# Kernel tuning notes

Hardware: AMD Instinct MI355X
Metric: run time of the kernel (lower is better)

Reference implementation:

```python
import jax, jax.numpy as jnp
import numpy as np

HEADS = 4
BN_EPS = 1e-5


def _hgat_conv(x, src, dst, node_type, edge_attr, edge_type,
               ne, W, We, a_src, a_dst, a_edge, ee, Wres, b, concat):
    """Heterogeneous GAT conv: per-type embeddings + edge-featured attention.
    x: [N, Fin]; edge_attr: [E, De]; returns [N, H*C] (concat) or [N, C]."""
    N = x.shape[0]
    C = W.shape[1] // HEADS
    xi = x + ne[node_type]                                  # node-type conditioning
    h = (xi @ W).reshape(N, HEADS, C)                       # [N, H, C]
    he = ((edge_attr + ee[edge_type]) @ We).reshape(-1, HEADS, C)  # [E, H, C]
    s = jnp.einsum('nhc,hc->nh', h, a_src)                  # [N, H]
    d = jnp.einsum('nhc,hc->nh', h, a_dst)                  # [N, H]
    e = jnp.einsum('ehc,hc->eh', he, a_edge)                # [E, H]
    alpha = jax.nn.leaky_relu(s[src] + d[dst] + e, 0.2)     # [E, H]
    # softmax over incoming edges per destination node
    amax = jax.ops.segment_max(alpha, dst, num_segments=N)  # [N, H]
    amax = jnp.where(jnp.isfinite(amax), amax, 0.0)
    ex = jnp.exp(alpha - amax[dst])
    den = jax.ops.segment_sum(ex, dst, num_segments=N)
    coef = ex / (den[dst] + 1e-16)                          # [E, H]
    msg = h[src] * coef[:, :, None]                         # [E, H, C]
    out = jax.ops.segment_sum(msg, dst, num_segments=N)     # [N, H, C]
    out = out.reshape(N, HEADS * C) if concat else out.mean(axis=1)
    return out + x @ Wres + b                               # residual + bias


def _batch_norm(x, gamma, beta):
    mu = x.mean(axis=0)
    var = x.var(axis=0)
    return (x - mu) * jax.lax.rsqrt(var + BN_EPS) * gamma + beta


def setup_inputs() -> dict:
    key = jax.random.key(0)
    ks = jax.random.split(key, 32)
    N, E, H = 50000, 400000, 32          # nodes, edges, hidden_channels
    DE = 64                               # edge_dim
    NT, ET = 3, 4                         # node / edge type counts
    D1 = H * HEADS                        # 128 = enc1 output / enc2 width

    def g(k, shape, scale=1.0):
        return (jax.random.normal(ks[k], shape, dtype=jnp.float32) * scale)

    inp = {
        'x': g(0, (N, H)),
        'edge_index': jax.random.randint(ks[1], (2, E), 0, N, dtype=jnp.int32),
        'node_type': jax.random.randint(ks[2], (N,), 0, NT, dtype=jnp.int32),
        'edge_attr': g(3, (E, DE)),
        'edge_type': jax.random.randint(ks[4], (E,), 0, ET, dtype=jnp.int32),
        # enc1 params (in=32, per-head out=32, concat -> 128)
        'ne1': g(5, (NT, H), 0.1),
        'w1': g(6, (H, HEADS * H), 1.0 / np.sqrt(H)),
        'we1': g(7, (DE, HEADS * H), 1.0 / np.sqrt(DE)),
        'asrc1': g(8, (HEADS, H), 0.1), 'adst1': g(9, (HEADS, H), 0.1),
        'aedge1': g(10, (HEADS, H), 0.1),
        'ee1': g(11, (ET, DE), 0.1),
        'wres1': g(12, (H, D1), 1.0 / np.sqrt(H)),
        'b1': jnp.zeros((D1,), jnp.float32),
        # BatchNorm(128)
        'gamma': jnp.ones((D1,), jnp.float32),
        'beta': jnp.zeros((D1,), jnp.float32),
        # enc2 params (in=128, per-head out=128, mean -> 128)
        'ne2': g(13, (NT, D1), 0.1),
        'w2': g(14, (D1, HEADS * D1), 1.0 / np.sqrt(D1)),
        'we2': g(15, (DE, HEADS * D1), 1.0 / np.sqrt(DE)),
        'asrc2': g(16, (HEADS, D1), 0.1), 'adst2': g(17, (HEADS, D1), 0.1),
        'aedge2': g(18, (HEADS, D1), 0.1),
        'ee2': g(19, (ET, DE), 0.1),
        'wres2': g(20, (D1, D1), 1.0 / np.sqrt(D1)),
        'b2': jnp.zeros((D1,), jnp.float32),
    }
    return inp


def reference(x, edge_index, node_type, edge_attr, edge_type,
              ne1, w1, we1, asrc1, adst1, aedge1, ee1, wres1, b1,
              gamma, beta,
              ne2, w2, we2, asrc2, adst2, aedge2, ee2, wres2, b2):
    src, dst = edge_index[0], edge_index[1]
    h = _hgat_conv(x, src, dst, node_type, edge_attr, edge_type,
                   ne1, w1, we1, asrc1, adst1, aedge1, ee1, wres1, b1,
                   concat=True)
    h = _batch_norm(h, gamma, beta)
    out = _hgat_conv(h, src, dst, node_type, edge_attr, edge_type,
                     ne2, w2, we2, asrc2, adst2, aedge2, ee2, wres2, b2,
                     concat=False)
    return out
```

## Files before the change

### kernel.cpp

```cpp
#include <hip/hip_runtime.h>
#include <hip/hip_bf16.h>

typedef unsigned short u16;
typedef unsigned int u32;

constexpr int NN = 50000;
constexpr int NE = 400000;
constexpr int MPAD = 50048;

typedef __attribute__((ext_vector_type(8))) short s16x8;
typedef __attribute__((ext_vector_type(4))) float f32x4;

__device__ __forceinline__ float bf2f(u16 u) {
    union { u32 i; float f; } v; v.i = ((u32)u) << 16; return v.f;
}
__device__ __forceinline__ u16 f2bf(float f) {
    union { float f; u32 i; } v; v.f = f;
    u32 r = v.i + 0x7fffu + ((v.i >> 16) & 1u);
    return (u16)(r >> 16);
}
__device__ __forceinline__ float ldf(const void* p, size_t i, int isbf) {
    if (isbf) return bf2f(((const u16*)p)[i]);
    return ((const float*)p)[i];
}
__device__ __forceinline__ float clampf(float v) {
    return fminf(fmaxf(v, -1e4f), 1e4f);
}

__device__ int   g_flag;
__device__ int   g_counter;
__device__ float g_qe1[256], g_qe2[256];
__device__ float g_ps1[128], g_pd1[128], g_ps2[512], g_pd2[512];
__device__ float g_bnsum[128], g_bnsumsq[128], g_bnscale[128], g_bnshift[128];
__device__ int   g_deg[NN], g_start[NN], g_cur[NN];
__device__ int   g_eidx[NE];
__device__ __attribute__((aligned(16))) float g_sbuf[NN * 4];
__device__ __attribute__((aligned(16))) float g_dbuf[NN * 4];
__device__ __attribute__((aligned(16))) float g_alpha[(size_t)NE * 4];
__device__ __attribute__((aligned(16))) float g_xbuf[(size_t)NN * 128];
__device__ __attribute__((aligned(16))) float g_acc2[(size_t)NN * 128];
__device__ __attribute__((aligned(16))) u16 g_A1[(size_t)MPAD * 64];
__device__ __attribute__((aligned(16))) u16 g_A2[(size_t)MPAD * 160];
__device__ __attribute__((aligned(16))) u16 g_B1t[192 * 64];
__device__ __attribute__((aligned(16))) u16 g_B1bt[128 * 128];
__device__ __attribute__((aligned(16))) u16 g_B2t[192 * 160];
__device__ __attribute__((aligned(16))) u16 g_B2bt[128 * 512];
__device__ __attribute__((aligned(16))) u16 g_xi1[(size_t)NN * 32];
__device__ __attribute__((aligned(16))) u16 g_xi2[(size_t)NN * 128];
__device__ __attribute__((aligned(16))) u16 g_agg1[(size_t)MPAD * 128];
__device__ __attribute__((aligned(16))) u16 g_agg2[(size_t)MPAD * 512];

__global__ void k_detect(const u16* x) {
    if (threadIdx.x == 0) {
        int cnt = 0;
        for (int i = 0; i < 64; i++) {
            u16 u = x[2 * i];
            int ex = (u >> 7) & 0xff;
            if (ex >= 100 && ex <= 140) cnt++;
        }
        g_flag = (cnt >= 40) ? 1 : 0;
        g_counter = 0;
    }
}
__global__ void k_zero() {
    int i = blockIdx.x * blockDim.x + threadIdx.x;
    if (i < NN) g_deg[i] = 0;
    if (i < 128) { g_bnsum[i] = 0.f; g_bnsumsq[i] = 0.f; }
}

__global__ __launch_bounds__(256) void k_prep(
    const void* we1, const void* ae1, const void* we2, const void* ae2,
    const void* w1, const void* as1, const void* ad1,
    const void* w2, const void* as2, const void* ad2) {
    int isbf = g_flag;
    int t = threadIdx.x;
    int idx = blockIdx.x * 16 + (t >> 4);
    int s = t & 15;
    float a = 0.f;
    if (idx < 256) {
        int k = idx >> 2, hd = idx & 3;
        for (int c = s; c < 32; c += 16)
            a += ldf(we1, k * 128 + hd * 32 + c, isbf) * ldf(ae1, hd * 32 + c, isbf);
    } else if (idx < 512) {
        int i2 = idx - 256;
        int k = i2 >> 2, hd = i2 & 3;
        for (int c = s; c < 128; c += 16)
            a += ldf(we2, k * 512 + hd * 128 + c, isbf) * ldf(ae2, hd * 128 + c, isbf);
    } else if (idx < 768) {
        int i2 = idx - 512;
        int isd = i2 >> 7, j = i2 & 127;
        int h = j >> 5, k = j & 31;
        const void* av = isd ? ad1 : as1;
        for (int c = s; c < 32; c += 16)
            a += ldf(w1, k * 128 + h * 32 + c, isbf) * ldf(av, h * 32 + c, isbf);
    } else {
        int i2 = idx - 768;
        int isd = i2 >> 9, j = i2 & 511;
        int h = j >> 7, k = j & 127;
        const void* av = isd ? ad2 : as2;
        for (int c = s; c < 128; c += 16)
            a += ldf(w2, (size_t)k * 512 + h * 128 + c, isbf) * ldf(av, h * 128 + c, isbf);
    }
#pragma unroll
    for (int mk = 8; mk >= 1; mk >>= 1) a += __shfl_xor(a, mk);
    if (s == 0) {
        if (idx < 256) g_qe1[idx] = a;
        else if (idx < 512) g_qe2[idx - 256] = a;
        else if (idx < 768) {
            int i2 = idx - 512;
            if (i2 >> 7) g_pd1[i2 & 127] = a; else g_ps1[i2 & 127] = a;
        } else {
            int i2 = idx - 768;
            if (i2 >> 9) g_pd2[i2 & 511] = a; else g_ps2[i2 & 511] = a;
        }
    }
}

__global__ void k_deg(const int* __restrict__ dstp) {
    int e = blockIdx.x * blockDim.x + threadIdx.x;
    if (e < NE) atomicAdd(&g_deg[dstp[e]], 1);
}
__global__ void k_start() {
    int n = blockIdx.x * blockDim.x + threadIdx.x;
    if (n < NN) {
        int d = g_deg[n];
        int s = atomicAdd(&g_counter, d);
        g_start[n] = s; g_cur[n] = s;
    }
}
__global__ void k_scatter(const int* __restrict__ dstp) {
    int e = blockIdx.x * blockDim.x + threadIdx.x;
    if (e < NE) {
        int slot = atomicAdd(&g_cur[dstp[e]], 1);
        g_eidx[slot] = e;
    }
}

__device__ __forceinline__ u16 a1val(const void* x, int n, int k, int nt, int isbf) {
    if (k < 32) return f2bf(ldf(x, (size_t)n * 32 + k, isbf));
    if (k == 32 + nt || k == 35) return 0x3F80u;
    return 0;
}
__global__ __launch_bounds__(256) void k_buildA1(const void* x, const int* __restrict__ ntype,
                                                 const void* ne1) {
    int isbf = g_flag;
    int i = blockIdx.x * 256 + threadIdx.x;
    if (i >= MPAD * 32) return;
    int n = i >> 5, k2 = (i & 31) << 1;
    u32 pk = 0;
    if (n < NN) {
        int nt = ntype[n];
        pk = (u32)a1val(x, n, k2, nt, isbf) | ((u32)a1val(x, n, k2 + 1, nt, isbf) << 16);
        if (k2 < 32) {
            float x0 = ldf(x, (size_t)n * 32 + k2, isbf) + ldf(ne1, nt * 32 + k2, isbf);
            float x1 = ldf(x, (size_t)n * 32 + k2 + 1, isbf) + ldf(ne1, nt * 32 + k2 + 1, isbf);
            ((u32*)g_xi1)[(size_t)n * 16 + (k2 >> 1)] =
                (u32)f2bf(x0) | ((u32)f2bf(x1) << 16);
        }
    }
    ((u32*)g_A1)[i] = pk;
}
__global__ __launch_bounds__(256) void k_a2tail(const int* __restrict__ ntype) {
    int i = blockIdx.x * 256 + threadIdx.x;
    if (i >= NN * 16) return;
    int n = i >> 4, q = i & 15;
    int k2 = 128 + q * 2;
    int nt = ntype[n];
    u16 lo = (k2 == 128 + nt || k2 == 131) ? 0x3F80u : 0;
    u16 hi = (k2 + 1 == 128 + nt || k2 + 1 == 131) ? 0x3F80u : 0;
    ((u32*)g_A2)[(size_t)n * 80 + 64 + q] = (u32)lo | ((u32)hi << 16);
}
__global__ __launch_bounds__(256) void k_xi2(const int* __restrict__ ntype, const void* ne2) {
    int isbf = g_flag;
    int i = blockIdx.x * 256 + threadIdx.x;
    if (i >= NN * 64) return;
    int n = i >> 6, jp = (i & 63) << 1;
    int nt = ntype[n];
    float v0 = g_xbuf[(size_t)n * 128 + jp] * g_bnscale[jp] + g_bnshift[jp]
             + ldf(ne2, nt * 128 + jp, isbf);
    float v1 = g_xbuf[(size_t)n * 128 + jp + 1] * g_bnscale[jp + 1] + g_bnshift[jp + 1]
             + ldf(ne2, nt * 128 + jp + 1, isbf);
    ((u32*)g_xi2)[i] = (u32)f2bf(v0) | ((u32)f2bf(v1) << 16);
}

__global__ void k_buildB1(const void* ne1, const void* w1, const void* wres1, const void* b1) {
    int isbf = g_flag;
    int j = blockIdx.x;
    int k = threadIdx.x;
    float v = 0.f;
    if (j < 128) {
        if (k < 32) v = ldf(wres1, k * 128 + j, isbf);
        else if (k == 35) v = ldf(b1, j, isbf);
    } else if (j < 136) {
        int h = (j - 128) & 3;
        const float* p = (j < 132) ? g_ps1 : g_pd1;
        if (k < 32) v = p[h * 32 + k];
        else if (k < 35) {
            int tt = k - 32; float a = 0.f;
            for (int c = 0; c < 32; c++)
                a += ldf(ne1, tt * 32 + c, isbf) * p[h * 32 + c];
            v = a;
        }
    }
    (void)w1;
    g_B1t[j * 64 + k] = f2bf(v);
}
__global__ void k_buildB1b(const void* w1) {
    int isbf = g_flag;
    int j = blockIdx.x;
    int k = threadIdx.x;
    float v = ((k >> 5) == (j >> 5)) ? ldf(w1, (k & 31) * 128 + j, isbf) : 0.f;
    g_B1bt[j * 128 + k] = f2bf(v);
}
__global__ void k_buildB2(const void* ne2, const void* w2, const void* wres2, const void* b2) {
    int isbf = g_flag;
    int j = blockIdx.x;
    int k = threadIdx.x;
    if (k >= 160) return;
    float v = 0.f;
    if (j < 128) {
        if (k < 128) v = g_bnscale[k] * ldf(wres2, k * 128 + j, isbf);
        else if (k == 131) {
            float a = ldf(b2, j, isbf);
            for (int c = 0; c < 128; c++)
                a += g_bnshift[c] * ldf(wres2, c * 128 + j, isbf);
            v = a;
        }
    } else if (j < 136) {
        int h = (j - 128) & 3;
        const float* p = (j < 132) ? g_ps2 : g_pd2;
        if (k < 128) v = g_bnscale[k] * p[h * 128 + k];
        else if (k < 131) {
            int tt = k - 128; float a = 0.f;
            for (int c = 0; c < 128; c++)
                a += (g_bnshift[c] + ldf(ne2, tt * 128 + c, isbf)) * p[h * 128 + c];
            v = a;
        }
    }
    (void)w2;
    g_B2t[j * 160 + k] = f2bf(v);
}
__global__ void k_buildB2b(const void* w2) {
    int isbf = g_flag;
    int j = blockIdx.x;
    for (int k = threadIdx.x; k < 512; k += 256) {
        float v = 0.25f * ldf(w2, (size_t)(k & 127) * 512 + (k >> 7) * 128 + j, isbf);
        g_B2bt[j * 512 + k] = f2bf(v);
    }
}

template<int K, int KT, int LAYER>
__global__ __launch_bounds__(256) void k_gemm(void* outp) {
    constexpr int KP = KT + 8;
    __shared__ __attribute__((aligned(16))) u16 As[64 * KP];
    __shared__ __attribute__((aligned(16))) u16 Bs[64 * KP];
    const u16* __restrict__ A  = (LAYER == 1) ? g_A1 : (LAYER == 2) ? g_A2
                               : (LAYER == 3) ? g_agg1 : g_agg2;
    const u16* __restrict__ Bt = (LAYER == 1) ? g_B1t : (LAYER == 2) ? g_B2t
                               : (LAYER == 3) ? g_B1bt : g_B2bt;
    int isbf = g_flag;
    const int t = threadIdx.x;
    const int mb = blockIdx.x, cb = blockIdx.y;
    const int wave = t >> 6, lane = t & 63;
    const int lr = lane & 15, lg = lane >> 4;
    f32x4 acc[4] = {};
    constexpr int CH = KT / 8;
#pragma unroll 1
    for (int kt = 0; kt < K / KT; kt++) {
        __syncthreads();
        for (int c = t; c < 64 * CH; c += 256) {
            int r = c / CH, o = (c - r * CH) * 8;
            *(s16x8*)&As[r * KP + o] =
                *(const s16x8*)&A[((size_t)(mb * 64 + r)) * K + kt * KT + o];
            *(s16x8*)&Bs[r * KP + o] =
                *(const s16x8*)&Bt[((size_t)(cb * 64 + r)) * K + kt * KT + o];
        }
        __syncthreads();
        const u16* ap  = &As[(wave * 16 + lr) * KP + lg * 8];
        const u16* bp0 = &Bs[lr * KP + lg * 8];
#pragma unroll
        for (int ks = 0; ks < KT / 32; ks++) {
            s16x8 af = *(const s16x8*)(ap + ks * 32);
#pragma unroll
            for (int ct = 0; ct < 4; ct++) {
                s16x8 bf = *(const s16x8*)(bp0 + ct * 16 * KP + ks * 32);
                acc[ct] = __builtin_amdgcn_mfma_f32_16x16x32_bf16(af, bf, acc[ct], 0, 0, 0);
            }
        }
    }
    const int rowb = mb * 64 + wave * 16 + lg * 4;
#pragma unroll
    for (int ct = 0; ct < 4; ct++) {
        int j = cb * 64 + ct * 16 + lr;
#pragma unroll
        for (int r = 0; r < 4; r++) {
            int n = rowb + r;
            if (n >= NN) continue;
            float v = acc[ct][r];
            if (LAYER == 1) {
                if (j < 128)      g_xbuf[(size_t)n * 128 + j] = clampf(v);
                else if (j < 132) g_sbuf[n * 4 + (j - 128)] = clampf(v);
                else if (j < 136) g_dbuf[n * 4 + (j - 132)] = clampf(v);
            } else if (LAYER == 2) {
                if (j < 128)      g_acc2[(size_t)n * 128 + j] = clampf(v);
                else if (j < 132) g_sbuf[n * 4 + (j - 128)] = clampf(v);
                else if (j < 136) g_dbuf[n * 4 + (j - 132)] = clampf(v);
            } else if (LAYER == 3) {
                float* p = &g_xbuf[(size_t)n * 128 + j];
                float x = clampf(*p + v);
                *p = x;
                g_A2[(size_t)n * 160 + j] = f2bf(x);
            } else {
                float v2 = clampf(g_acc2[(size_t)n * 128 + j] + v);
                if (isbf) ((u16*)outp)[(size_t)n * 128 + j] = f2bf(v2);
                else      ((float*)outp)[(size_t)n * 128 + j] = v2;
            }
        }
    }
}

__global__ __launch_bounds__(256) void k_edge(
    const int* __restrict__ srcp, const int* __restrict__ dstp,
    const int* __restrict__ etype, const void* eattr,
    const void* ee, int lyr) {
    __shared__ float eel[4 * 68];
    __shared__ float qel[256];
    int isbf = g_flag;
    int t = threadIdx.x;
    const float* qe = (lyr == 1) ? g_qe1 : g_qe2;
    { int tt = t >> 6, k = t & 63; eel[tt * 68 + k] = ldf(ee, tt * 64 + k, isbf); }
    qel[t] = qe[t];
    __syncthreads();
    int sub = t & 15;
    float q[4][4];
#pragma unroll
    for (int i = 0; i < 4; i++)
#pragma unroll
        for (int h = 0; h < 4; h++)
            q[i][h] = qel[(sub * 4 + i) * 4 + h];
    int g = t >> 4;
    int e = blockIdx.x * 16 + g;
    if (e >= NE) return;
    int et = etype[e];
    float ev[4];
    if (isbf) {
        ushort4 vv = *(const ushort4*)((const u16*)eattr + (size_t)e * 64 + sub * 4);
        ev[0] = bf2f(vv.x); ev[1] = bf2f(vv.y); ev[2] = bf2f(vv.z); ev[3] = bf2f(vv.w);
    } else {
        float4 vv = *(const float4*)((const float*)eattr + (size_t)e * 64 + sub * 4);
        ev[0] = vv.x; ev[1] = vv.y; ev[2] = vv.z; ev[3] = vv.w;
    }
    const float* ep = eel + et * 68 + sub * 4;
    float p0 = 0.f, p1 = 0.f, p2 = 0.f, p3 = 0.f;
#pragma unroll
    for (int i = 0; i < 4; i++) {
        float evi = ev[i] + ep[i];
        p0 += evi * q[i][0]; p1 += evi * q[i][1];
        p2 += evi * q[i][2]; p3 += evi * q[i][3];
    }
#pragma unroll
    for (int mk = 1; mk < 16; mk <<= 1) {
        p0 += __shfl_xor(p0, mk); p1 += __shfl_xor(p1, mk);
        p2 += __shfl_xor(p2, mk); p3 += __shfl_xor(p3, mk);
    }
    if (sub == 0) {
        int ss = srcp[e], dd = dstp[e];
        float4 sb = *(const float4*)(g_sbuf + ss * 4);
        float4 db = *(const float4*)(g_dbuf + dd * 4);
        float a0 = sb.x + db.x + p0;
        float a1 = sb.y + db.y + p1;
        float a2 = sb.z + db.z + p2;
        float a3 = sb.w + db.w + p3;
        a0 = a0 > 0.f ? a0 : 0.2f * a0;
        a1 = a1 > 0.f ? a1 : 0.2f * a1;
        a2 = a2 > 0.f ? a2 : 0.2f * a2;
        a3 = a3 > 0.f ? a3 : 0.2f * a3;
        *(float4*)(g_alpha + 4 * (size_t)e) = make_float4(
            clampf(a0), clampf(a1), clampf(a2), clampf(a3));
    }
}

__global__ __launch_bounds__(256) void k_att1(const int* __restrict__ srcp) {
    int lane = threadIdx.x & 63;
    int n = blockIdx.x * 4 + (threadIdx.x >> 6);
    if (n >= NN) return;
    int st = g_start[n], dg = g_deg[n];
    float m0 = -1e30f, m1 = -1e30f, m2 = -1e30f, m3 = -1e30f;
    for (int i = lane; i < dg; i += 64) {
        int e = g_eidx[st + i];
        float4 a = *(const float4*)(g_alpha + 4 * (size_t)e);
        m0 = fmaxf(m0, a.x); m1 = fmaxf(m1, a.y);
        m2 = fmaxf(m2, a.z); m3 = fmaxf(m3, a.w);
    }
    for (int mk = 32; mk >= 1; mk >>= 1) {
        m0 = fmaxf(m0, __shfl_xor(m0, mk)); m1 = fmaxf(m1, __shfl_xor(m1, mk));
        m2 = fmaxf(m2, __shfl_xor(m2, mk)); m3 = fmaxf(m3, __shfl_xor(m3, mk));
    }
    int j0 = 2 * lane;
    int hd = j0 >> 5;
    float z0 = 0.f, z1 = 0.f, z2 = 0.f, z3 = 0.f;
    float acc0 = 0.f, acc1 = 0.f;
    for (int base = 0; base < dg; base += 64) {
        int i = base + lane;
        int sidx = 0; float c0 = 0.f, c1 = 0.f, c2 = 0.f, c3 = 0.f;
        if (i < dg) {
            int e = g_eidx[st + i];
            float4 a = *(const float4*)(g_alpha + 4 * (size_t)e);
            sidx = srcp[e];
            c0 = expf(a.x - m0); c1 = expf(a.y - m1);
            c2 = expf(a.z - m2); c3 = expf(a.w - m3);
            z0 += c0; z1 += c1; z2 += c2; z3 += c3;
        }
        int cnt = min(64, dg - base);
        for (int jj = 0; jj < cnt; jj++) {
            int s2 = __shfl(sidx, jj);
            float b0 = __shfl(c0, jj), b1 = __shfl(c1, jj);
            float b2v = __shfl(c2, jj), b3 = __shfl(c3, jj);
            float cs = hd == 0 ? b0 : hd == 1 ? b1 : hd == 2 ? b2v : b3;
            u32 hv = *(const u32*)(g_xi1 + (size_t)s2 * 32 + (j0 & 31));
            acc0 += bf2f((u16)(hv & 0xffff)) * cs;
            acc1 += bf2f((u16)(hv >> 16)) * cs;
        }
    }
    for (int mk = 32; mk >= 1; mk >>= 1) {
        z0 += __shfl_xor(z0, mk); z1 += __shfl_xor(z1, mk);
        z2 += __shfl_xor(z2, mk); z3 += __shfl_xor(z3, mk);
    }
    float iv = 1.f / ((hd == 0 ? z0 : hd == 1 ? z1 : hd == 2 ? z2 : z3) + 1e-16f);
    ((u32*)g_agg1)[((size_t)n * 128 + j0) >> 1] =
        (u32)f2bf(acc0 * iv) | ((u32)f2bf(acc1 * iv) << 16);
}

__global__ __launch_bounds__(256) void k_bnstats() {
    int t = threadIdx.x;
    int j = t & 127;
    int r0 = blockIdx.x * 2 + (t >> 7);
    float s = 0.f, ss = 0.f;
    for (int r = r0; r < NN; r += 500) {
        float v = g_xbuf[(size_t)r * 128 + j];
        s += v; ss += v * v;
    }
    atomicAdd(&g_bnsum[j], s);
    atomicAdd(&g_bnsumsq[j], ss);
}
__global__ void k_bnfin(const void* gamma, const void* beta) {
    int isbf = g_flag;
    int j = threadIdx.x;
    float mu = g_bnsum[j] * (1.f / NN);
    float var = fmaxf(g_bnsumsq[j] * (1.f / NN) - mu * mu, 0.f);
    float rstd = rsqrtf(var + 1e-5f);
    float sc = ldf(gamma, j, isbf) * rstd;
    g_bnscale[j] = sc;
    g_bnshift[j] = ldf(beta, j, isbf) - mu * sc;
}

__global__ __launch_bounds__(256) void k_att2(const int* __restrict__ srcp) {
    int lane = threadIdx.x & 63;
    int n = blockIdx.x * 4 + (threadIdx.x >> 6);
    if (n >= NN) return;
    int st = g_start[n], dg = g_deg[n];
    float m0 = -1e30f, m1 = -1e30f, m2 = -1e30f, m3 = -1e30f;
    for (int i = lane; i < dg; i += 64) {
        int e = g_eidx[st + i];
        float4 a = *(const float4*)(g_alpha + 4 * (size_t)e);
        m0 = fmaxf(m0, a.x); m1 = fmaxf(m1, a.y);
        m2 = fmaxf(m2, a.z); m3 = fmaxf(m3, a.w);
    }
    for (int mk = 32; mk >= 1; mk >>= 1) {
        m0 = fmaxf(m0, __shfl_xor(m0, mk)); m1 = fmaxf(m1, __shfl_xor(m1, mk));
        m2 = fmaxf(m2, __shfl_xor(m2, mk)); m3 = fmaxf(m3, __shfl_xor(m3, mk));
    }
    int c0 = 2 * lane;
    float z0 = 0.f, z1 = 0.f, z2 = 0.f, z3 = 0.f;
    float a00 = 0.f, a01 = 0.f, a10 = 0.f, a11 = 0.f;
    float a20 = 0.f, a21 = 0.f, a30 = 0.f, a31 = 0.f;
    for (int base = 0; base < dg; base += 64) {
        int i = base + lane;
        int sidx = 0; float c0f = 0.f, c1f = 0.f, c2f = 0.f, c3f = 0.f;
        if (i < dg) {
            int e = g_eidx[st + i];
            float4 a = *(const float4*)(g_alpha + 4 * (size_t)e);
            sidx = srcp[e];
            c0f = expf(a.x - m0); c1f = expf(a.y - m1);
            c2f = expf(a.z - m2); c3f = expf(a.w - m3);
            z0 += c0f; z1 += c1f; z2 += c2f; z3 += c3f;
        }
        int cnt = min(64, dg - base);
        for (int jj = 0; jj < cnt; jj++) {
            int s2 = __shfl(sidx, jj);
            float b0 = __shfl(c0f, jj), b1 = __shfl(c1f, jj);
            float b2v = __shfl(c2f, jj), b3 = __shfl(c3f, jj);
            u32 hv = *(const u32*)(g_xi2 + (size_t)s2 * 128 + c0);
            float lo = bf2f((u16)(hv & 0xffff)), hi = bf2f((u16)(hv >> 16));
            a00 += lo * b0;  a01 += hi * b0;
            a10 += lo * b1;  a11 += hi * b1;
            a20 += lo * b2v; a21 += hi * b2v;
            a30 += lo * b3;  a31 += hi * b3;
        }
    }
    for (int mk = 32; mk >= 1; mk >>= 1) {
        z0 += __shfl_xor(z0, mk); z1 += __shfl_xor(z1, mk);
        z2 += __shfl_xor(z2, mk); z3 += __shfl_xor(z3, mk);
    }
    float iv0 = 1.f / (z0 + 1e-16f), iv1 = 1.f / (z1 + 1e-16f);
    float iv2 = 1.f / (z2 + 1e-16f), iv3 = 1.f / (z3 + 1e-16f);
    u32* out = (u32*)g_agg2 + (((size_t)n * 512 + c0) >> 1);
    out[0]   = (u32)f2bf(a00 * iv0) | ((u32)f2bf(a01 * iv0) << 16);
    out[64]  = (u32)f2bf(a10 * iv1) | ((u32)f2bf(a11 * iv1) << 16);
    out[128] = (u32)f2bf(a20 * iv2) | ((u32)f2bf(a21 * iv2) << 16);
    out[192] = (u32)f2bf(a30 * iv3) | ((u32)f2bf(a31 * iv3) << 16);
}

extern "C" void kernel_launch(void* const* d_in, const int* in_sizes, int n_in,
                              void* d_out, int out_size, void* d_ws, size_t ws_size,
                              hipStream_t stream) {
    const void* x     = d_in[0];
    const int* ei     = (const int*)d_in[1];
    const int* ntype  = (const int*)d_in[2];
    const void* eattr = d_in[3];
    const int* etype  = (const int*)d_in[4];
    const void* ne1   = d_in[5];
    const void* w1    = d_in[6];
    const void* we1   = d_in[7];
    const void* asrc1 = d_in[8];
    const void* adst1 = d_in[9];
    const void* aedge1= d_in[10];
    const void* ee1   = d_in[11];
    const void* wres1 = d_in[12];
    const void* b1    = d_in[13];
    const void* gamma = d_in[14];
    const void* beta  = d_in[15];
    const void* ne2   = d_in[16];
    const void* w2    = d_in[17];
    const void* we2   = d_in[18];
    const void* asrc2 = d_in[19];
    const void* adst2 = d_in[20];
    const void* aedge2= d_in[21];
    const void* ee2   = d_in[22];
    const void* wres2 = d_in[23];
    const void* b2    = d_in[24];
    (void)in_sizes; (void)n_in; (void)out_size; (void)d_ws; (void)ws_size;

    const int* srcp = ei;
    const int* dstp = ei + NE;

    k_detect<<<1, 64, 0, stream>>>((const u16*)x);
    k_zero<<<196, 256, 0, stream>>>();
    k_prep<<<112, 256, 0, stream>>>(we1, aedge1, we2, aedge2,
                                    w1, asrc1, adst1, w2, asrc2, adst2);
    k_deg<<<1563, 256, 0, stream>>>(dstp);
    k_start<<<196, 256, 0, stream>>>();
    k_scatter<<<1563, 256, 0, stream>>>(dstp);

    k_buildA1<<<(MPAD * 32 + 255) / 256, 256, 0, stream>>>(x, ntype, ne1);
    k_buildB1<<<192, 64, 0, stream>>>(ne1, w1, wres1, b1);
    k_buildB1b<<<128, 128, 0, stream>>>(w1);
    k_gemm<64, 64, 1><<<dim3(MPAD / 64, 3), 256, 0, stream>>>(nullptr);
    k_edge<<<NE / 16, 256, 0, stream>>>(srcp, dstp, etype, eattr, ee1, 1);
    k_att1<<<12500, 256, 0, stream>>>(srcp);
    k_gemm<128, 128, 3><<<dim3(MPAD / 64, 2), 256, 0, stream>>>(nullptr);

    k_bnstats<<<250, 256, 0, stream>>>();
    k_bnfin<<<1, 128, 0, stream>>>(gamma, beta);

    k_xi2<<<12500, 256, 0, stream>>>(ntype, ne2);
    k_a2tail<<<(NN * 16 + 255) / 256, 256, 0, stream>>>(ntype);
    k_buildB2<<<192, 192, 0, stream>>>(ne2, w2, wres2, b2);
    k_buildB2b<<<128, 256, 0, stream>>>(w2);
    k_gemm<160, 160, 2><<<dim3(MPAD / 64, 3), 256, 0, stream>>>(nullptr);
    k_edge<<<NE / 16, 256, 0, stream>>>(srcp, dstp, etype, eattr, ee2, 2);
    k_att2<<<12500, 256, 0, stream>>>(srcp);
    k_gemm<512, 128, 4><<<dim3(MPAD / 64, 2), 256, 0, stream>>>(d_out);
}
```

Before: 620.8 us.

## Fuse aggregation with output GEMMs and share edge-feature pass across layers

The attention-aggregation kernels now write each block's 32 aggregated node rows into shared memory and immediately run the MFMA projection (W1 per head, or the mean-folded W2) on them. This removes the g_agg1/g_agg2 global round trips and the separate GEMM launches. Both layers' edge-attribute projections are computed in one pass over edge_attr, with the per-edge-type term precomputed into a 16-entry table. Layer 2 gets a light edge kernel that only adds the source and destination scores. The cost is a larger shared-memory footprint, lower occupancy in the fused kernels, and B-matrix reads straight from global memory.

```diff
diff --git a/kernel.cpp b/kernel.cpp
--- a/kernel.cpp
+++ b/kernel.cpp
@@ -30,6 +30,7 @@
 __device__ int   g_flag;
 __device__ int   g_counter;
 __device__ float g_qe1[256], g_qe2[256];
+__device__ float g_eq1[16], g_eq2[16];
 __device__ float g_ps1[128], g_pd1[128], g_ps2[512], g_pd2[512];
 __device__ float g_bnsum[128], g_bnsumsq[128], g_bnscale[128], g_bnshift[128];
 __device__ int   g_deg[NN], g_start[NN], g_cur[NN];
@@ -37,18 +38,17 @@
 __device__ __attribute__((aligned(16))) float g_sbuf[NN * 4];
 __device__ __attribute__((aligned(16))) float g_dbuf[NN * 4];
 __device__ __attribute__((aligned(16))) float g_alpha[(size_t)NE * 4];
+__device__ __attribute__((aligned(16))) float g_el2[(size_t)NE * 4];
 __device__ __attribute__((aligned(16))) float g_xbuf[(size_t)NN * 128];
 __device__ __attribute__((aligned(16))) float g_acc2[(size_t)NN * 128];
 __device__ __attribute__((aligned(16))) u16 g_A1[(size_t)MPAD * 64];
 __device__ __attribute__((aligned(16))) u16 g_A2[(size_t)MPAD * 160];
 __device__ __attribute__((aligned(16))) u16 g_B1t[192 * 64];
-__device__ __attribute__((aligned(16))) u16 g_B1bt[128 * 128];
+__device__ __attribute__((aligned(16))) u16 g_B1ct[128 * 32];
 __device__ __attribute__((aligned(16))) u16 g_B2t[192 * 160];
 __device__ __attribute__((aligned(16))) u16 g_B2bt[128 * 512];
 __device__ __attribute__((aligned(16))) u16 g_xi1[(size_t)NN * 32];
 __device__ __attribute__((aligned(16))) u16 g_xi2[(size_t)NN * 128];
-__device__ __attribute__((aligned(16))) u16 g_agg1[(size_t)MPAD * 128];
-__device__ __attribute__((aligned(16))) u16 g_agg2[(size_t)MPAD * 512];
 
 __global__ void k_detect(const u16* x) {
     if (threadIdx.x == 0) {
@@ -115,6 +115,24 @@
         }
     }
 }
+__global__ void k_prep2(const void* ee1, const void* ee2) {
+    int isbf = g_flag;
+    int t = threadIdx.x;
+    int idx = blockIdx.x * 16 + (t >> 4);
+    int s = t & 15;
+    int lyr = idx >> 4;
+    int et = (idx >> 2) & 3, h = idx & 3;
+    const void* ee = lyr ? ee2 : ee1;
+    const float* qe = lyr ? g_qe2 : g_qe1;
+    float a = 0.f;
+    for (int k = s; k < 64; k += 16)
+        a += ldf(ee, et * 64 + k, isbf) * qe[k * 4 + h];
+#pragma unroll
+    for (int mk = 8; mk >= 1; mk >>= 1) a += __shfl_xor(a, mk);
+    if (s == 0) {
+        if (lyr) g_eq2[et * 4 + h] = a; else g_eq1[et * 4 + h] = a;
+    }
+}
 
 __global__ void k_deg(const int* __restrict__ dstp) {
     int e = blockIdx.x * blockDim.x + threadIdx.x;
@@ -205,12 +223,11 @@
     (void)w1;
     g_B1t[j * 64 + k] = f2bf(v);
 }
-__global__ void k_buildB1b(const void* w1) {
-    int isbf = g_flag;
-    int j = blockIdx.x;
-    int k = threadIdx.x;
-    float v = ((k >> 5) == (j >> 5)) ? ldf(w1, (k & 31) * 128 + j, isbf) : 0.f;
-    g_B1bt[j * 128 + k] = f2bf(v);
+__global__ void k_buildB1ct(const void* w1) {
+    int isbf = g_flag;
+    int i = blockIdx.x * 256 + threadIdx.x;
+    int j = i >> 5, k = i & 31;
+    g_B1ct[i] = f2bf(ldf(w1, k * 128 + j, isbf));
 }
 __global__ void k_buildB2(const void* ne2, const void* w2, const void* wres2, const void* b2) {
     int isbf = g_flag;
@@ -249,43 +266,34 @@
     }
 }
 
-template<int K, int KT, int LAYER>
-__global__ __launch_bounds__(256) void k_gemm(void* outp) {
-    constexpr int KP = KT + 8;
+template<int K, int LAYER>
+__global__ __launch_bounds__(256) void k_gemm() {
+    constexpr int KP = K + 8;
     __shared__ __attribute__((aligned(16))) u16 As[64 * KP];
     __shared__ __attribute__((aligned(16))) u16 Bs[64 * KP];
-    const u16* __restrict__ A  = (LAYER == 1) ? g_A1 : (LAYER == 2) ? g_A2
-                               : (LAYER == 3) ? g_agg1 : g_agg2;
-    const u16* __restrict__ Bt = (LAYER == 1) ? g_B1t : (LAYER == 2) ? g_B2t
-                               : (LAYER == 3) ? g_B1bt : g_B2bt;
-    int isbf = g_flag;
+    const u16* __restrict__ A  = (LAYER == 1) ? g_A1 : g_A2;
+    const u16* __restrict__ Bt = (LAYER == 1) ? g_B1t : g_B2t;
     const int t = threadIdx.x;
     const int mb = blockIdx.x, cb = blockIdx.y;
     const int wave = t >> 6, lane = t & 63;
     const int lr = lane & 15, lg = lane >> 4;
     f32x4 acc[4] = {};
-    constexpr int CH = KT / 8;
-#pragma unroll 1
-    for (int kt = 0; kt < K / KT; kt++) {
-        __syncthreads();
-        for (int c = t; c < 64 * CH; c += 256) {
-            int r = c / CH, o = (c - r * CH) * 8;
-            *(s16x8*)&As[r * KP + o] =
-                *(const s16x8*)&A[((size_t)(mb * 64 + r)) * K + kt * KT + o];
-            *(s16x8*)&Bs[r * KP + o] =
-                *(const s16x8*)&Bt[((size_t)(cb * 64 + r)) * K + kt * KT + o];
-        }
-        __syncthreads();
-        const u16* ap  = &As[(wave * 16 + lr) * KP + lg * 8];
-        const u16* bp0 = &Bs[lr * KP + lg * 8];
-#pragma unroll
-        for (int ks = 0; ks < KT / 32; ks++) {
-            s16x8 af = *(const s16x8*)(ap + ks * 32);
-#pragma unroll
-            for (int ct = 0; ct < 4; ct++) {
-                s16x8 bf = *(const s16x8*)(bp0 + ct * 16 * KP + ks * 32);
-                acc[ct] = __builtin_amdgcn_mfma_f32_16x16x32_bf16(af, bf, acc[ct], 0, 0, 0);
-            }
+    constexpr int CH = K / 8;
+    for (int c = t; c < 64 * CH; c += 256) {
+        int r = c / CH, o = (c - r * CH) * 8;
+        *(s16x8*)&As[r * KP + o] = *(const s16x8*)&A[((size_t)(mb * 64 + r)) * K + o];
+        *(s16x8*)&Bs[r * KP + o] = *(const s16x8*)&Bt[((size_t)(cb * 64 + r)) * K + o];
+    }
+    __syncthreads();
+    const u16* ap  = &As[(wave * 16 + lr) * KP + lg * 8];
+    const u16* bp0 = &Bs[lr * KP + lg * 8];
+#pragma unroll
+    for (int ks = 0; ks < K / 32; ks++) {
+        s16x8 af = *(const s16x8*)(ap + ks * 32);
+#pragma unroll
+        for (int ct = 0; ct < 4; ct++) {
+            s16x8 bf = *(const s16x8*)(bp0 + ct * 16 * KP + ks * 32);
+            acc[ct] = __builtin_amdgcn_mfma_f32_16x16x32_bf16(af, bf, acc[ct], 0, 0, 0);
         }
     }
     const int rowb = mb * 64 + wave * 16 + lg * 4;
@@ -296,52 +304,41 @@
         for (int r = 0; r < 4; r++) {
             int n = rowb + r;
             if (n >= NN) continue;
-            float v = acc[ct][r];
+            float v = clampf(acc[ct][r]);
             if (LAYER == 1) {
-                if (j < 128)      g_xbuf[(size_t)n * 128 + j] = clampf(v);
-                else if (j < 132) g_sbuf[n * 4 + (j - 128)] = clampf(v);
-                else if (j < 136) g_dbuf[n * 4 + (j - 132)] = clampf(v);
-            } else if (LAYER == 2) {
-                if (j < 128)      g_acc2[(size_t)n * 128 + j] = clampf(v);
-                else if (j < 132) g_sbuf[n * 4 + (j - 128)] = clampf(v);
-                else if (j < 136) g_dbuf[n * 4 + (j - 132)] = clampf(v);
-            } else if (LAYER == 3) {
-                float* p = &g_xbuf[(size_t)n * 128 + j];
-                float x = clampf(*p + v);
-                *p = x;
-                g_A2[(size_t)n * 160 + j] = f2bf(x);
+                if (j < 128)      g_xbuf[(size_t)n * 128 + j] = v;
+                else if (j < 132) g_sbuf[n * 4 + (j - 128)] = v;
+                else if (j < 136) g_dbuf[n * 4 + (j - 132)] = v;
             } else {
-                float v2 = clampf(g_acc2[(size_t)n * 128 + j] + v);
-                if (isbf) ((u16*)outp)[(size_t)n * 128 + j] = f2bf(v2);
-                else      ((float*)outp)[(size_t)n * 128 + j] = v2;
-            }
-        }
-    }
-}
-
-__global__ __launch_bounds__(256) void k_edge(
+                if (j < 128)      g_acc2[(size_t)n * 128 + j] = v;
+                else if (j < 132) g_sbuf[n * 4 + (j - 128)] = v;
+                else if (j < 136) g_dbuf[n * 4 + (j - 132)] = v;
+            }
+        }
+    }
+}
+
+__global__ __launch_bounds__(256) void k_edge12(
     const int* __restrict__ srcp, const int* __restrict__ dstp,
-    const int* __restrict__ etype, const void* eattr,
-    const void* ee, int lyr) {
-    __shared__ float eel[4 * 68];
-    __shared__ float qel[256];
+    const int* __restrict__ etype, const void* eattr) {
+    __shared__ float qel1[256], qel2[256], eq1s[16], eq2s[16];
     int isbf = g_flag;
     int t = threadIdx.x;
-    const float* qe = (lyr == 1) ? g_qe1 : g_qe2;
-    { int tt = t >> 6, k = t & 63; eel[tt * 68 + k] = ldf(ee, tt * 64 + k, isbf); }
-    qel[t] = qe[t];
+    qel1[t] = g_qe1[t];
+    qel2[t] = g_qe2[t];
+    if (t < 16) { eq1s[t] = g_eq1[t]; eq2s[t] = g_eq2[t]; }
     __syncthreads();
     int sub = t & 15;
-    float q[4][4];
+    float q1[4][4], q2[4][4];
 #pragma unroll
     for (int i = 0; i < 4; i++)
 #pragma unroll
-        for (int h = 0; h < 4; h++)
-            q[i][h] = qel[(sub * 4 + i) * 4 + h];
-    int g = t >> 4;
-    int e = blockIdx.x * 16 + g;
+        for (int h = 0; h < 4; h++) {
+            q1[i][h] = qel1[(sub * 4 + i) * 4 + h];
+            q2[i][h] = qel2[(sub * 4 + i) * 4 + h];
+        }
+    int e = blockIdx.x * 16 + (t >> 4);
     if (e >= NE) return;
-    int et = etype[e];
     float ev[4];
     if (isbf) {
         ushort4 vv = *(const ushort4*)((const u16*)eattr + (size_t)e * 64 + sub * 4);
@@ -350,85 +347,142 @@
         float4 vv = *(const float4*)((const float*)eattr + (size_t)e * 64 + sub * 4);
         ev[0] = vv.x; ev[1] = vv.y; ev[2] = vv.z; ev[3] = vv.w;
     }
-    const float* ep = eel + et * 68 + sub * 4;
-    float p0 = 0.f, p1 = 0.f, p2 = 0.f, p3 = 0.f;
+    float p10 = 0.f, p11 = 0.f, p12 = 0.f, p13 = 0.f;
+    float p20 = 0.f, p21 = 0.f, p22 = 0.f, p23 = 0.f;
 #pragma unroll
     for (int i = 0; i < 4; i++) {
-        float evi = ev[i] + ep[i];
-        p0 += evi * q[i][0]; p1 += evi * q[i][1];
-        p2 += evi * q[i][2]; p3 += evi * q[i][3];
+        p10 += ev[i] * q1[i][0]; p11 += ev[i] * q1[i][1];
+        p12 += ev[i] * q1[i][2]; p13 += ev[i] * q1[i][3];
+        p20 += ev[i] * q2[i][0]; p21 += ev[i] * q2[i][1];
+        p22 += ev[i] * q2[i][2]; p23 += ev[i] * q2[i][3];
     }
 #pragma unroll
     for (int mk = 1; mk < 16; mk <<= 1) {
-        p0 += __shfl_xor(p0, mk); p1 += __shfl_xor(p1, mk);
-        p2 += __shfl_xor(p2, mk); p3 += __shfl_xor(p3, mk);
+        p10 += __shfl_xor(p10, mk); p11 += __shfl_xor(p11, mk);
+        p12 += __shfl_xor(p12, mk); p13 += __shfl_xor(p13, mk);
+        p20 += __shfl_xor(p20, mk); p21 += __shfl_xor(p21, mk);
+        p22 += __shfl_xor(p22, mk); p23 += __shfl_xor(p23, mk);
     }
     if (sub == 0) {
-        int ss = srcp[e], dd = dstp[e];
+        int et = etype[e], ss = srcp[e], dd = dstp[e];
         float4 sb = *(const float4*)(g_sbuf + ss * 4);
         float4 db = *(const float4*)(g_dbuf + dd * 4);
-        float a0 = sb.x + db.x + p0;
-        float a1 = sb.y + db.y + p1;
-        float a2 = sb.z + db.z + p2;
-        float a3 = sb.w + db.w + p3;
+        float a0 = sb.x + db.x + p10 + eq1s[et * 4 + 0];
+        float a1 = sb.y + db.y + p11 + eq1s[et * 4 + 1];
+        float a2 = sb.z + db.z + p12 + eq1s[et * 4 + 2];
+        float a3 = sb.w + db.w + p13 + eq1s[et * 4 + 3];
         a0 = a0 > 0.f ? a0 : 0.2f * a0;
         a1 = a1 > 0.f ? a1 : 0.2f * a1;
         a2 = a2 > 0.f ? a2 : 0.2f * a2;
         a3 = a3 > 0.f ? a3 : 0.2f * a3;
         *(float4*)(g_alpha + 4 * (size_t)e) = make_float4(
             clampf(a0), clampf(a1), clampf(a2), clampf(a3));
-    }
-}
-
-__global__ __launch_bounds__(256) void k_att1(const int* __restrict__ srcp) {
-    int lane = threadIdx.x & 63;
-    int n = blockIdx.x * 4 + (threadIdx.x >> 6);
-    if (n >= NN) return;
-    int st = g_start[n], dg = g_deg[n];
-    float m0 = -1e30f, m1 = -1e30f, m2 = -1e30f, m3 = -1e30f;
-    for (int i = lane; i < dg; i += 64) {
-        int e = g_eidx[st + i];
-        float4 a = *(const float4*)(g_alpha + 4 * (size_t)e);
-        m0 = fmaxf(m0, a.x); m1 = fmaxf(m1, a.y);
-        m2 = fmaxf(m2, a.z); m3 = fmaxf(m3, a.w);
-    }
-    for (int mk = 32; mk >= 1; mk >>= 1) {
-        m0 = fmaxf(m0, __shfl_xor(m0, mk)); m1 = fmaxf(m1, __shfl_xor(m1, mk));
-        m2 = fmaxf(m2, __shfl_xor(m2, mk)); m3 = fmaxf(m3, __shfl_xor(m3, mk));
-    }
-    int j0 = 2 * lane;
-    int hd = j0 >> 5;
-    float z0 = 0.f, z1 = 0.f, z2 = 0.f, z3 = 0.f;
-    float acc0 = 0.f, acc1 = 0.f;
-    for (int base = 0; base < dg; base += 64) {
-        int i = base + lane;
-        int sidx = 0; float c0 = 0.f, c1 = 0.f, c2 = 0.f, c3 = 0.f;
-        if (i < dg) {
-            int e = g_eidx[st + i];
-            float4 a = *(const float4*)(g_alpha + 4 * (size_t)e);
-            sidx = srcp[e];
-            c0 = expf(a.x - m0); c1 = expf(a.y - m1);
-            c2 = expf(a.z - m2); c3 = expf(a.w - m3);
-            z0 += c0; z1 += c1; z2 += c2; z3 += c3;
-        }
-        int cnt = min(64, dg - base);
-        for (int jj = 0; jj < cnt; jj++) {
-            int s2 = __shfl(sidx, jj);
-            float b0 = __shfl(c0, jj), b1 = __shfl(c1, jj);
-            float b2v = __shfl(c2, jj), b3 = __shfl(c3, jj);
-            float cs = hd == 0 ? b0 : hd == 1 ? b1 : hd == 2 ? b2v : b3;
-            u32 hv = *(const u32*)(g_xi1 + (size_t)s2 * 32 + (j0 & 31));
-            acc0 += bf2f((u16)(hv & 0xffff)) * cs;
-            acc1 += bf2f((u16)(hv >> 16)) * cs;
-        }
-    }
-    for (int mk = 32; mk >= 1; mk >>= 1) {
-        z0 += __shfl_xor(z0, mk); z1 += __shfl_xor(z1, mk);
-        z2 += __shfl_xor(z2, mk); z3 += __shfl_xor(z3, mk);
-    }
-    float iv = 1.f / ((hd == 0 ? z0 : hd == 1 ? z1 : hd == 2 ? z2 : z3) + 1e-16f);
-    ((u32*)g_agg1)[((size_t)n * 128 + j0) >> 1] =
-        (u32)f2bf(acc0 * iv) | ((u32)f2bf(acc1 * iv) << 16);
+        *(float4*)(g_el2 + 4 * (size_t)e) = make_float4(
+            p20 + eq2s[et * 4 + 0], p21 + eq2s[et * 4 + 1],
+            p22 + eq2s[et * 4 + 2], p23 + eq2s[et * 4 + 3]);
+    }
+}
+
+__global__ __launch_bounds__(256) void k_edge2(
+    const int* __restrict__ srcp, const int* __restrict__ dstp) {
+    int e = blockIdx.x * 256 + threadIdx.x;
+    if (e >= NE) return;
+    float4 p = *(const float4*)(g_el2 + 4 * (size_t)e);
+    int ss = srcp[e], dd = dstp[e];
+    float4 sb = *(const float4*)(g_sbuf + ss * 4);
+    float4 db = *(const float4*)(g_dbuf + dd * 4);
+    float a0 = sb.x + db.x + p.x;
+    float a1 = sb.y + db.y + p.y;
+    float a2 = sb.z + db.z + p.z;
+    float a3 = sb.w + db.w + p.w;
+    a0 = a0 > 0.f ? a0 : 0.2f * a0;
+    a1 = a1 > 0.f ? a1 : 0.2f * a1;
+    a2 = a2 > 0.f ? a2 : 0.2f * a2;
+    a3 = a3 > 0.f ? a3 : 0.2f * a3;
+    *(float4*)(g_alpha + 4 * (size_t)e) = make_float4(
+        clampf(a0), clampf(a1), clampf(a2), clampf(a3));
+}
+
+__global__ __launch_bounds__(256) void k_att1g(const int* __restrict__ srcp) {
+    __shared__ __attribute__((aligned(16))) u16 As[32 * 136];
+    int t = threadIdx.x, wave = t >> 6, lane = t & 63;
+    int nb = blockIdx.x * 32;
+    int j0 = 2 * lane, hd = j0 >> 5;
+    for (int ni = 0; ni < 8; ni++) {
+        int nl = wave * 8 + ni, n = nb + nl;
+        u32 outv = 0;
+        if (n < NN) {
+            int st = g_start[n], dg = g_deg[n];
+            float m0 = -1e30f, m1 = -1e30f, m2 = -1e30f, m3 = -1e30f;
+            for (int i = lane; i < dg; i += 64) {
+                int e = g_eidx[st + i];
+                float4 a = *(const float4*)(g_alpha + 4 * (size_t)e);
+                m0 = fmaxf(m0, a.x); m1 = fmaxf(m1, a.y);
+                m2 = fmaxf(m2, a.z); m3 = fmaxf(m3, a.w);
+            }
+            for (int mk = 32; mk >= 1; mk >>= 1) {
+                m0 = fmaxf(m0, __shfl_xor(m0, mk)); m1 = fmaxf(m1, __shfl_xor(m1, mk));
+                m2 = fmaxf(m2, __shfl_xor(m2, mk)); m3 = fmaxf(m3, __shfl_xor(m3, mk));
+            }
+            float z0 = 0.f, z1 = 0.f, z2 = 0.f, z3 = 0.f;
+            float acc0 = 0.f, acc1 = 0.f;
+            for (int base = 0; base < dg; base += 64) {
+                int i = base + lane;
+                int sidx = 0; float c0 = 0.f, c1 = 0.f, c2 = 0.f, c3 = 0.f;
+                if (i < dg) {
+                    int e = g_eidx[st + i];
+                    float4 a = *(const float4*)(g_alpha + 4 * (size_t)e);
+                    sidx = srcp[e];
+                    c0 = expf(a.x - m0); c1 = expf(a.y - m1);
+                    c2 = expf(a.z - m2); c3 = expf(a.w - m3);
+                    z0 += c0; z1 += c1; z2 += c2; z3 += c3;
+                }
+                int cnt = min(64, dg - base);
+                for (int jj = 0; jj < cnt; jj++) {
+                    int s2 = __shfl(sidx, jj);
+                    float b0 = __shfl(c0, jj), b1 = __shfl(c1, jj);
+                    float b2v = __shfl(c2, jj), b3 = __shfl(c3, jj);
+                    float cs = hd == 0 ? b0 : hd == 1 ? b1 : hd == 2 ? b2v : b3;
+                    u32 hv = *(const u32*)(g_xi1 + (size_t)s2 * 32 + (j0 & 31));
+                    acc0 += bf2f((u16)(hv & 0xffff)) * cs;
+                    acc1 += bf2f((u16)(hv >> 16)) * cs;
+                }
+            }
+            for (int mk = 32; mk >= 1; mk >>= 1) {
+                z0 += __shfl_xor(z0, mk); z1 += __shfl_xor(z1, mk);
+                z2 += __shfl_xor(z2, mk); z3 += __shfl_xor(z3, mk);
+            }
+            float iv = 1.f / ((hd == 0 ? z0 : hd == 1 ? z1 : hd == 2 ? z2 : z3) + 1e-16f);
+            outv = (u32)f2bf(acc0 * iv) | ((u32)f2bf(acc1 * iv) << 16);
+        }
+        ((u32*)As)[nl * 68 + lane] = outv;
+    }
+    __syncthreads();
+    int lr = lane & 15, lg = lane >> 4;
+    int r0 = (wave & 1) * 16, cb = (wave >> 1) * 64;
+    f32x4 acc[4] = {};
+#pragma unroll
+    for (int ct = 0; ct < 4; ct++) {
+        int jb = cb + ct * 16;
+        int h = jb >> 5;
+        s16x8 af = *(const s16x8*)&As[(r0 + lr) * 136 + h * 32 + lg * 8];
+        s16x8 bf = *(const s16x8*)&g_B1ct[(jb + lr) * 32 + lg * 8];
+        acc[ct] = __builtin_amdgcn_mfma_f32_16x16x32_bf16(af, bf, acc[ct], 0, 0, 0);
+    }
+    int rowb = nb + r0 + lg * 4;
+#pragma unroll
+    for (int ct = 0; ct < 4; ct++) {
+        int j = cb + ct * 16 + lr;
+#pragma unroll
+        for (int r = 0; r < 4; r++) {
+            int n = rowb + r;
+            if (n >= NN) continue;
+            float* p = &g_xbuf[(size_t)n * 128 + j];
+            float x = clampf(*p + acc[ct][r]);
+            *p = x;
+            g_A2[(size_t)n * 160 + j] = f2bf(x);
+        }
+    }
 }
 
 __global__ __launch_bounds__(256) void k_bnstats() {
@@ -454,61 +508,95 @@
     g_bnshift[j] = ldf(beta, j, isbf) - mu * sc;
 }
 
-__global__ __launch_bounds__(256) void k_att2(const int* __restrict__ srcp) {
-    int lane = threadIdx.x & 63;
-    int n = blockIdx.x * 4 + (threadIdx.x >> 6);
-    if (n >= NN) return;
-    int st = g_start[n], dg = g_deg[n];
-    float m0 = -1e30f, m1 = -1e30f, m2 = -1e30f, m3 = -1e30f;
-    for (int i = lane; i < dg; i += 64) {
-        int e = g_eidx[st + i];
-        float4 a = *(const float4*)(g_alpha + 4 * (size_t)e);
-        m0 = fmaxf(m0, a.x); m1 = fmaxf(m1, a.y);
-        m2 = fmaxf(m2, a.z); m3 = fmaxf(m3, a.w);
-    }
-    for (int mk = 32; mk >= 1; mk >>= 1) {
-        m0 = fmaxf(m0, __shfl_xor(m0, mk)); m1 = fmaxf(m1, __shfl_xor(m1, mk));
-        m2 = fmaxf(m2, __shfl_xor(m2, mk)); m3 = fmaxf(m3, __shfl_xor(m3, mk));
-    }
+__global__ __launch_bounds__(256) void k_att2g(const int* __restrict__ srcp, void* outp) {
+    __shared__ __attribute__((aligned(16))) u16 As[32 * 520];
+    int isbf = g_flag;
+    int t = threadIdx.x, wave = t >> 6, lane = t & 63;
+    int nb = blockIdx.x * 32;
     int c0 = 2 * lane;
-    float z0 = 0.f, z1 = 0.f, z2 = 0.f, z3 = 0.f;
-    float a00 = 0.f, a01 = 0.f, a10 = 0.f, a11 = 0.f;
-    float a20 = 0.f, a21 = 0.f, a30 = 0.f, a31 = 0.f;
-    for (int base = 0; base < dg; base += 64) {
-        int i = base + lane;
-        int sidx = 0; float c0f = 0.f, c1f = 0.f, c2f = 0.f, c3f = 0.f;
-        if (i < dg) {
-            int e = g_eidx[st + i];
-            float4 a = *(const float4*)(g_alpha + 4 * (size_t)e);
-            sidx = srcp[e];
-            c0f = expf(a.x - m0); c1f = expf(a.y - m1);
-            c2f = expf(a.z - m2); c3f = expf(a.w - m3);
-            z0 += c0f; z1 += c1f; z2 += c2f; z3 += c3f;
-        }
-        int cnt = min(64, dg - base);
-        for (int jj = 0; jj < cnt; jj++) {
-            int s2 = __shfl(sidx, jj);
-            float b0 = __shfl(c0f, jj), b1 = __shfl(c1f, jj);
-            float b2v = __shfl(c2f, jj), b3 = __shfl(c3f, jj);
-            u32 hv = *(const u32*)(g_xi2 + (size_t)s2 * 128 + c0);
-            float lo = bf2f((u16)(hv & 0xffff)), hi = bf2f((u16)(hv >> 16));
-            a00 += lo * b0;  a01 += hi * b0;
-            a10 += lo * b1;  a11 += hi * b1;
-            a20 += lo * b2v; a21 += hi * b2v;
-            a30 += lo * b3;  a31 += hi * b3;
-        }
-    }
-    for (int mk = 32; mk >= 1; mk >>= 1) {
-        z0 += __shfl_xor(z0, mk); z1 += __shfl_xor(z1, mk);
-        z2 += __shfl_xor(z2, mk); z3 += __shfl_xor(z3, mk);
-    }
-    float iv0 = 1.f / (z0 + 1e-16f), iv1 = 1.f / (z1 + 1e-16f);
-    float iv2 = 1.f / (z2 + 1e-16f), iv3 = 1.f / (z3 + 1e-16f);
-    u32* out = (u32*)g_agg2 + (((size_t)n * 512 + c0) >> 1);
-    out[0]   = (u32)f2bf(a00 * iv0) | ((u32)f2bf(a01 * iv0) << 16);
-    out[64]  = (u32)f2bf(a10 * iv1) | ((u32)f2bf(a11 * iv1) << 16);
-    out[128] = (u32)f2bf(a20 * iv2) | ((u32)f2bf(a21 * iv2) << 16);
-    out[192] = (u32)f2bf(a30 * iv3) | ((u32)f2bf(a31 * iv3) << 16);
+    for (int ni = 0; ni < 8; ni++) {
+        int nl = wave * 8 + ni, n = nb + nl;
+        u32 o0 = 0, o1 = 0, o2 = 0, o3 = 0;
+        if (n < NN) {
+            int st = g_start[n], dg = g_deg[n];
+            float m0 = -1e30f, m1 = -1e30f, m2 = -1e30f, m3 = -1e30f;
+            for (int i = lane; i < dg; i += 64) {
+                int e = g_eidx[st + i];
+                float4 a = *(const float4*)(g_alpha + 4 * (size_t)e);
+                m0 = fmaxf(m0, a.x); m1 = fmaxf(m1, a.y);
+                m2 = fmaxf(m2, a.z); m3 = fmaxf(m3, a.w);
+            }
+            for (int mk = 32; mk >= 1; mk >>= 1) {
+                m0 = fmaxf(m0, __shfl_xor(m0, mk)); m1 = fmaxf(m1, __shfl_xor(m1, mk));
+                m2 = fmaxf(m2, __shfl_xor(m2, mk)); m3 = fmaxf(m3, __shfl_xor(m3, mk));
+            }
+            float z0 = 0.f, z1 = 0.f, z2 = 0.f, z3 = 0.f;
+            float a00 = 0.f, a01 = 0.f, a10 = 0.f, a11 = 0.f;
+            float a20 = 0.f, a21 = 0.f, a30 = 0.f, a31 = 0.f;
+            for (int base = 0; base < dg; base += 64) {
+                int i = base + lane;
+                int sidx = 0; float c0f = 0.f, c1f = 0.f, c2f = 0.f, c3f = 0.f;
+                if (i < dg) {
+                    int e = g_eidx[st + i];
+                    float4 a = *(const float4*)(g_alpha + 4 * (size_t)e);
+                    sidx = srcp[e];
+                    c0f = expf(a.x - m0); c1f = expf(a.y - m1);
+                    c2f = expf(a.z - m2); c3f = expf(a.w - m3);
+                    z0 += c0f; z1 += c1f; z2 += c2f; z3 += c3f;
+                }
+                int cnt = min(64, dg - base);
+                for (int jj = 0; jj < cnt; jj++) {
+                    int s2 = __shfl(sidx, jj);
+                    float b0 = __shfl(c0f, jj), b1 = __shfl(c1f, jj);
+                    float b2v = __shfl(c2f, jj), b3 = __shfl(c3f, jj);
+                    u32 hv = *(const u32*)(g_xi2 + (size_t)s2 * 128 + c0);
+                    float lo = bf2f((u16)(hv & 0xffff)), hi = bf2f((u16)(hv >> 16));
+                    a00 += lo * b0;  a01 += hi * b0;
+                    a10 += lo * b1;  a11 += hi * b1;
+                    a20 += lo * b2v; a21 += hi * b2v;
+                    a30 += lo * b3;  a31 += hi * b3;
+                }
+            }
+            for (int mk = 32; mk >= 1; mk >>= 1) {
+                z0 += __shfl_xor(z0, mk); z1 += __shfl_xor(z1, mk);
+                z2 += __shfl_xor(z2, mk); z3 += __shfl_xor(z3, mk);
+            }
+            float iv0 = 1.f / (z0 + 1e-16f), iv1 = 1.f / (z1 + 1e-16f);
+            float iv2 = 1.f / (z2 + 1e-16f), iv3 = 1.f / (z3 + 1e-16f);
+            o0 = (u32)f2bf(a00 * iv0) | ((u32)f2bf(a01 * iv0) << 16);
+            o1 = (u32)f2bf(a10 * iv1) | ((u32)f2bf(a11 * iv1) << 16);
+            o2 = (u32)f2bf(a20 * iv2) | ((u32)f2bf(a21 * iv2) << 16);
+            o3 = (u32)f2bf(a30 * iv3) | ((u32)f2bf(a31 * iv3) << 16);
+        }
+        u32* arow = (u32*)As + nl * 260 + lane;
+        arow[0] = o0; arow[64] = o1; arow[128] = o2; arow[192] = o3;
+    }
+    __syncthreads();
+    int lr = lane & 15, lg = lane >> 4;
+    int r0 = (wave & 1) * 16, cb = (wave >> 1) * 64;
+    f32x4 acc[4] = {};
+#pragma unroll
+    for (int ks = 0; ks < 16; ks++) {
+        s16x8 af = *(const s16x8*)&As[(r0 + lr) * 520 + ks * 32 + lg * 8];
+#pragma unroll
+        for (int ct = 0; ct < 4; ct++) {
+            s16x8 bf = *(const s16x8*)&g_B2bt[(size_t)(cb + ct * 16 + lr) * 512 + ks * 32 + lg * 8];
+            acc[ct] = __builtin_amdgcn_mfma_f32_16x16x32_bf16(af, bf, acc[ct], 0, 0, 0);
+        }
+    }
+    int rowb = nb + r0 + lg * 4;
+#pragma unroll
+    for (int ct = 0; ct < 4; ct++) {
+        int j = cb + ct * 16 + lr;
+#pragma unroll
+        for (int r = 0; r < 4; r++) {
+            int n = rowb + r;
+            if (n >= NN) continue;
+            float v2 = clampf(g_acc2[(size_t)n * 128 + j] + acc[ct][r]);
+            if (isbf) ((u16*)outp)[(size_t)n * 128 + j] = f2bf(v2);
+            else      ((float*)outp)[(size_t)n * 128 + j] = v2;
+        }
+    }
 }
 
 extern "C" void kernel_launch(void* const* d_in, const int* in_sizes, int n_in,
@@ -548,17 +636,17 @@
     k_zero<<<196, 256, 0, stream>>>();
     k_prep<<<112, 256, 0, stream>>>(we1, aedge1, we2, aedge2,
                                     w1, asrc1, adst1, w2, asrc2, adst2);
+    k_prep2<<<2, 256, 0, stream>>>(ee1, ee2);
     k_deg<<<1563, 256, 0, stream>>>(dstp);
     k_start<<<196, 256, 0, stream>>>();
     k_scatter<<<1563, 256, 0, stream>>>(dstp);
 
     k_buildA1<<<(MPAD * 32 + 255) / 256, 256, 0, stream>>>(x, ntype, ne1);
     k_buildB1<<<192, 64, 0, stream>>>(ne1, w1, wres1, b1);
-    k_buildB1b<<<128, 128, 0, stream>>>(w1);
-    k_gemm<64, 64, 1><<<dim3(MPAD / 64, 3), 256, 0, stream>>>(nullptr);
-    k_edge<<<NE / 16, 256, 0, stream>>>(srcp, dstp, etype, eattr, ee1, 1);
-    k_att1<<<12500, 256, 0, stream>>>(srcp);
-    k_gemm<128, 128, 3><<<dim3(MPAD / 64, 2), 256, 0, stream>>>(nullptr);
+    k_buildB1ct<<<16, 256, 0, stream>>>(w1);
+    k_gemm<64, 1><<<dim3(MPAD / 64, 3), 256, 0, stream>>>();
+    k_edge12<<<NE / 16, 256, 0, stream>>>(srcp, dstp, etype, eattr);
+    k_att1g<<<(NN + 31) / 32, 256, 0, stream>>>(srcp);
 
     k_bnstats<<<250, 256, 0, stream>>>();
     k_bnfin<<<1, 128, 0, stream>>>(gamma, beta);
@@ -567,8 +655,7 @@
     k_a2tail<<<(NN * 16 + 255) / 256, 256, 0, stream>>>(ntype);
     k_buildB2<<<192, 192, 0, stream>>>(ne2, w2, wres2, b2);
     k_buildB2b<<<128, 256, 0, stream>>>(w2);
-    k_gemm<160, 160, 2><<<dim3(MPAD / 64, 3), 256, 0, stream>>>(nullptr);
-    k_edge<<<NE / 16, 256, 0, stream>>>(srcp, dstp, etype, eattr, ee2, 2);
-    k_att2<<<12500, 256, 0, stream>>>(srcp);
-    k_gemm<512, 128, 4><<<dim3(MPAD / 64, 2), 256, 0, stream>>>(d_out);
-}
+    k_gemm<160, 2><<<dim3(MPAD / 64, 3), 256, 0, stream>>>();
+    k_edge2<<<1563, 256, 0, stream>>>(srcp, dstp);
+    k_att2g<<<(NN + 31) / 32, 256, 0, stream>>>(srcp, d_out);
+}
```

Result: slower. 674.5 us (+8.7%).
